# Performance work log

Hardware: AMD Instinct MI355X
Metric: run time of the kernel (lower is better)

The kernel has to match this reference:

```python
import jax, jax.numpy as jnp
import numpy as np

B, T, C, H = 2, 2048, 768, 12
HD = C // H  # head dim = 64
EPS = 1e-5


def layer_norm(x, g, b):
    mu = jnp.mean(x, axis=-1, keepdims=True)
    var = jnp.var(x, axis=-1, keepdims=True)
    return (x - mu) * jax.lax.rsqrt(var + EPS) * g + b


def setup_inputs() -> dict:
    key = jax.random.key(0)
    ks = jax.random.split(key, 5)
    s = 0.02
    return {
        "x": jax.random.normal(ks[0], (B, T, C), jnp.float32),
        "ln1_g": jnp.ones((C,), jnp.float32),
        "ln1_b": jnp.zeros((C,), jnp.float32),
        "W_qkv": jax.random.normal(ks[1], (C, 3 * C), jnp.float32) * s,
        "W_attn_proj": jax.random.normal(ks[2], (C, C), jnp.float32) * s,
        "ln2_g": jnp.ones((C,), jnp.float32),
        "ln2_b": jnp.zeros((C,), jnp.float32),
        "W_fc": jax.random.normal(ks[3], (C, 4 * C), jnp.float32) * s,
        "W_mlp_proj": jax.random.normal(ks[4], (4 * C, C), jnp.float32) * s,
    }


def attention(x, W_qkv, W_attn_proj):
    b, t, c = x.shape
    qkv = x @ W_qkv  # [B,T,3C]
    q, k, v = jnp.split(qkv, 3, axis=-1)
    # [B,H,T,HD]
    q = q.reshape(b, t, H, HD).transpose(0, 2, 1, 3)
    k = k.reshape(b, t, H, HD).transpose(0, 2, 1, 3)
    v = v.reshape(b, t, H, HD).transpose(0, 2, 1, 3)
    att = jnp.einsum("bhqd,bhkd->bhqk", q, k) * (1.0 / np.sqrt(HD).astype(np.float32))
    causal = jnp.tril(jnp.ones((t, t), jnp.bool_))
    att = jnp.where(causal, att, jnp.finfo(att.dtype).min)
    att = jax.nn.softmax(att, axis=-1)
    y = jnp.einsum("bhqk,bhkd->bhqd", att, v)
    y = y.transpose(0, 2, 1, 3).reshape(b, t, c)
    return y @ W_attn_proj


def mlp(x, W_fc, W_mlp_proj):
    h = jax.nn.gelu(x @ W_fc, approximate=False)
    return h @ W_mlp_proj


def reference(x, ln1_g, ln1_b, W_qkv, W_attn_proj, ln2_g, ln2_b, W_fc, W_mlp_proj):
    x = x + attention(layer_norm(x, ln1_g, ln1_b), W_qkv, W_attn_proj)
    x = x + mlp(layer_norm(x, ln2_g, ln2_b), W_fc, W_mlp_proj)
    return x
```

## Files before the change

kernel.cpp:

```cpp
#include <hip/hip_runtime.h>
#include <cstdint>
#include <cstddef>

typedef unsigned short u16;
typedef __attribute__((ext_vector_type(4))) float f32x4;
typedef __attribute__((ext_vector_type(8))) short bf16x8;

__device__ __forceinline__ u16 f2bf(float f) {
  unsigned int u = __builtin_bit_cast(unsigned int, f);
  u += 0x7fffu + ((u >> 16) & 1u);
  return (u16)(u >> 16);
}

__device__ __forceinline__ void gl_lds16(const u16* g, u16* lds_base) {
  __builtin_amdgcn_global_load_lds(
      (const __attribute__((address_space(1))) unsigned int*)g,
      (__attribute__((address_space(3))) unsigned int*)lds_base, 16, 0, 0);
}

__global__ __launch_bounds__(256) void transpose_all(const float* __restrict__ s0,
                                                     const float* __restrict__ s1,
                                                     const float* __restrict__ s2,
                                                     const float* __restrict__ s3,
                                                     u16* __restrict__ d0,
                                                     u16* __restrict__ d1,
                                                     u16* __restrict__ d2,
                                                     u16* __restrict__ d3) {
  __shared__ float tile[32][33];
  int idx = blockIdx.x;
  const float* src; u16* dst; int K, N, t;
  if (idx < 1728)      { src = s0; dst = d0; K = 768;  N = 2304; t = idx; }
  else if (idx < 2304) { src = s1; dst = d1; K = 768;  N = 768;  t = idx - 1728; }
  else if (idx < 4608) { src = s2; dst = d2; K = 768;  N = 3072; t = idx - 2304; }
  else                 { src = s3; dst = d3; K = 3072; N = 768;  t = idx - 4608; }
  int nt_n = N >> 5;
  int n0 = (t % nt_n) * 32, k0 = (t / nt_n) * 32;
  int tx = threadIdx.x & 31, ty = threadIdx.x >> 5;
#pragma unroll
  for (int i = 0; i < 4; ++i)
    tile[ty + i * 8][tx] = src[(size_t)(k0 + ty + i * 8) * N + n0 + tx];
  __syncthreads();
#pragma unroll
  for (int i = 0; i < 4; ++i)
    dst[(size_t)(n0 + ty + i * 8) * K + k0 + tx] = f2bf(tile[tx][ty + i * 8]);
}

__global__ __launch_bounds__(256) void transpose_v(const u16* __restrict__ qkvb,
                                                   u16* __restrict__ vt,
                                                   unsigned int* __restrict__ ctr) {
  __shared__ u16 tile[64 * 72];
  if (blockIdx.x == 0 && blockIdx.y == 0 && threadIdx.x == 0) *ctr = 0u;
  int t0 = blockIdx.x * 64;
  int bh = blockIdx.y;
  int b = bh / 12, h = bh % 12;
  int tid = threadIdx.x;
  int c8 = tid & 7, r = tid >> 3;
#pragma unroll
  for (int i = 0; i < 2; ++i) {
    int rr = r + i * 32;
    *(uint4*)&tile[rr * 72 + c8 * 8] =
        *(const uint4*)&qkvb[(size_t)(b * 2048 + t0 + rr) * 2304 + 1536 + h * 64 + c8 * 8];
  }
  __syncthreads();
#pragma unroll
  for (int i = 0; i < 2; ++i) {
    int dr = r + i * 32;
    u16 tmp[8];
#pragma unroll
    for (int j = 0; j < 8; ++j) tmp[j] = tile[(c8 * 8 + j) * 72 + dr];
    *(uint4*)&vt[((size_t)bh * 64 + dr) * 2048 + t0 + c8 * 8] = *(uint4*)tmp;
  }
}

__global__ __launch_bounds__(192) void ln_rows(const float* __restrict__ x,
                                               const float* __restrict__ g,
                                               const float* __restrict__ bb,
                                               u16* __restrict__ out) {
  int row = blockIdx.x;
  int t = threadIdx.x;
  float4 v = *(const float4*)(x + (size_t)row * 768 + t * 4);
  float s = v.x + v.y + v.z + v.w;
  float sq = v.x * v.x + v.y * v.y + v.z * v.z + v.w * v.w;
#pragma unroll
  for (int o = 32; o > 0; o >>= 1) {
    s += __shfl_down(s, o);
    sq += __shfl_down(sq, o);
  }
  __shared__ float ss[3], s2[3];
  int w = t >> 6;
  if ((t & 63) == 0) { ss[w] = s; s2[w] = sq; }
  __syncthreads();
  s = ss[0] + ss[1] + ss[2];
  sq = s2[0] + s2[1] + s2[2];
  float mu = s * (1.f / 768.f);
  float var = sq * (1.f / 768.f) - mu * mu;
  float rs = rsqrtf(var + 1e-5f);
  float4 gv = *(const float4*)(g + t * 4);
  float4 bv = *(const float4*)(bb + t * 4);
  u16 o4[4];
  o4[0] = f2bf((v.x - mu) * rs * gv.x + bv.x);
  o4[1] = f2bf((v.y - mu) * rs * gv.y + bv.y);
  o4[2] = f2bf((v.z - mu) * rs * gv.z + bv.z);
  o4[3] = f2bf((v.w - mu) * rs * gv.w + bv.w);
  *(uint2*)(out + (size_t)row * 768 + t * 4) = *(uint2*)o4;
}

template <int EPI, int CFG>
__global__ __launch_bounds__(256, (CFG == 0) ? 2 : 3)
void gemm_bt(const u16* __restrict__ A, const u16* __restrict__ BT,
             int M, int N, int K,
             float* __restrict__ outF, u16* __restrict__ outB,
             const float* __restrict__ res) {
  constexpr int TM = (CFG == 0) ? 128 : 64;
  constexpr int TN = (CFG == 0) ? 128 : 64;
  constexpr int MT = (CFG == 0) ? 4 : 1;
  __shared__ __align__(16) u16 Al[2][TM * 64];
  __shared__ __align__(16) u16 Bl[2][TN * 64];
  int tid = threadIdx.x;
  int lane = tid & 63, w = tid >> 6;
  int l16 = lane & 15, quad = lane >> 4;
  int swz = l16 & 7;
  int wrow = (CFG == 0) ? (w >> 1) * 64 : w * 16;
  int wcol = (CFG == 0) ? (w & 1) * 64 : 0;
  size_t rowA0 = (size_t)blockIdx.y * TM;
  size_t rowB0 = (size_t)blockIdx.x * TN;

  auto stage = [&](int buf, int k0) {
#pragma unroll
    for (int i = 0; i < TM / 32; ++i) {
      int cbase = (i * 4 + w) * 64;
      int chunk = cbase + lane;
      int r = chunk >> 3, c8 = (chunk & 7) ^ (r & 7);
      gl_lds16(&A[(rowA0 + r) * (size_t)K + k0 + c8 * 8], &Al[buf][cbase * 8]);
    }
#pragma unroll
    for (int i = 0; i < TN / 32; ++i) {
      int cbase = (i * 4 + w) * 64;
      int chunk = cbase + lane;
      int r = chunk >> 3, c8 = (chunk & 7) ^ (r & 7);
      gl_lds16(&BT[(rowB0 + r) * (size_t)K + k0 + c8 * 8], &Bl[buf][cbase * 8]);
    }
  };

  f32x4 acc[MT][4] = {};
  stage(0, 0);
  int cur = 0;
  for (int k0 = 0; k0 < K; k0 += 64) {
    __syncthreads();
    if (k0 + 64 < K) stage(cur ^ 1, k0 + 64);
#pragma unroll
    for (int ks = 0; ks < 2; ++ks) {
      int c = ks * 4 + quad;
      bf16x8 af[MT], bf[4];
#pragma unroll
      for (int mt = 0; mt < MT; ++mt)
        af[mt] = *(const bf16x8*)&Al[cur][(wrow + mt * 16 + l16) * 64 + (c ^ swz) * 8];
#pragma unroll
      for (int nt = 0; nt < 4; ++nt)
        bf[nt] = *(const bf16x8*)&Bl[cur][(wcol + nt * 16 + l16) * 64 + (c ^ swz) * 8];
#pragma unroll
      for (int mt = 0; mt < MT; ++mt)
#pragma unroll
        for (int nt = 0; nt < 4; ++nt)
          acc[mt][nt] = __builtin_amdgcn_mfma_f32_16x16x32_bf16(af[mt], bf[nt], acc[mt][nt], 0, 0, 0);
    }
    cur ^= 1;
  }

#pragma unroll
  for (int mt = 0; mt < MT; ++mt) {
#pragma unroll
    for (int i = 0; i < 4; ++i) {
      size_t row = rowA0 + wrow + mt * 16 + quad * 4 + i;
#pragma unroll
      for (int nt = 0; nt < 4; ++nt) {
        size_t col = rowB0 + wcol + nt * 16 + l16;
        float v = acc[mt][nt][i];
        if (EPI == 0) {
          outB[row * N + col] = f2bf(v);
        } else if (EPI == 1) {
          outF[row * N + col] = res[row * N + col] + v;
        } else {
          float ge = 0.5f * v * (1.f + erff(v * 0.70710678118654752f));
          outB[row * N + col] = f2bf(ge);
        }
      }
    }
  }
}

__global__ __launch_bounds__(256, 3) void flash_attn(const u16* __restrict__ qkv,
                                                     const u16* __restrict__ vt,
                                                     u16* __restrict__ y,
                                                     unsigned int* __restrict__ ctr) {
  __shared__ __align__(16) u16 Kl[2][64 * 64];
  __shared__ __align__(16) u16 Vl[2][64 * 64];
  __shared__ __align__(16) u16 Pl[4][16 * 72];
  __shared__ unsigned int s_unit;

  int tid = threadIdx.x;
  int lane = tid & 63, w = tid >> 6;
  int l16 = lane & 15, quad = lane >> 4;
  int swz = l16 & 7;
  u16* Pw = &Pl[w][0];
  const float sc = 0.125f * 1.44269504088896340736f;

  for (;;) {
    __syncthreads();
    if (tid == 0) s_unit = atomicAdd(ctr, 1u);
    __syncthreads();
    unsigned int u = s_unit;
    if (u >= 768u) return;

    int qt = 31 - (int)(u / 24u);
    int bh = (int)(u % 24u);
    int b = bh / 12, h = bh % 12;
    int qw = qt * 64 + w * 16;

    const u16* base = qkv + (size_t)b * 2048 * 2304;
    const u16* vbase = vt + (size_t)bh * 64 * 2048;

    auto stage = [&](int buf, int t0) {
#pragma unroll
      for (int i = 0; i < 2; ++i) {
        int cbase = (i * 4 + w) * 64;
        int chunk = cbase + lane;
        int r = chunk >> 3, c8 = (chunk & 7) ^ (r & 7);
        gl_lds16(base + (size_t)(t0 + r) * 2304 + 768 + h * 64 + c8 * 8, &Kl[buf][cbase * 8]);
      }
#pragma unroll
      for (int i = 0; i < 2; ++i) {
        int cbase = (i * 4 + w) * 64;
        int chunk = cbase + lane;
        int r = chunk >> 3, c8 = (chunk & 7) ^ (r & 7);
        gl_lds16(vbase + (size_t)r * 2048 + t0 + c8 * 8, &Vl[buf][cbase * 8]);
      }
    };

    bf16x8 qf0, qf1;
    {
      const u16* qp = base + (size_t)(qw + l16) * 2304 + h * 64 + quad * 8;
      qf0 = *(const bf16x8*)qp;
      qf1 = *(const bf16x8*)(qp + 32);
    }

    f32x4 O[4] = {};
    float l_i[4] = {0.f, 0.f, 0.f, 0.f};

    int nkb = qt + 1;
    stage(0, 0);
    int cur = 0;
    for (int kb = 0; kb < nkb; ++kb) {
      int kt0 = kb << 6;
      __syncthreads();
      if (kb + 1 < nkb) stage(cur ^ 1, kt0 + 64);

      f32x4 S[4];
#pragma unroll
      for (int nt = 0; nt < 4; ++nt) {
        bf16x8 k0 = *(const bf16x8*)&Kl[cur][(nt * 16 + l16) * 64 + (quad ^ swz) * 8];
        bf16x8 k1 = *(const bf16x8*)&Kl[cur][(nt * 16 + l16) * 64 + ((4 + quad) ^ swz) * 8];
        f32x4 z = {};
        z = __builtin_amdgcn_mfma_f32_16x16x32_bf16(qf0, k0, z, 0, 0, 0);
        S[nt] = __builtin_amdgcn_mfma_f32_16x16x32_bf16(qf1, k1, z, 0, 0, 0);
      }

      bool diag = (kb == nkb - 1);
#pragma unroll
      for (int nt = 0; nt < 4; ++nt) {
        int tk = kt0 + nt * 16 + l16;
#pragma unroll
        for (int i = 0; i < 4; ++i) {
          float p = exp2f(S[nt][i] * sc);
          if (diag && tk > qw + quad * 4 + i) p = 0.f;
          l_i[i] += p;
          Pw[(quad * 4 + i) * 72 + nt * 16 + l16] =
              (u16)(__builtin_bit_cast(unsigned int, p) >> 16);
        }
      }

      asm volatile("s_waitcnt lgkmcnt(0)" ::: "memory");

#pragma unroll
      for (int c = 0; c < 2; ++c) {
        bf16x8 pf = *(const bf16x8*)&Pw[l16 * 72 + c * 32 + quad * 8];
#pragma unroll
        for (int dt = 0; dt < 4; ++dt) {
          bf16x8 vf = *(const bf16x8*)&Vl[cur][(dt * 16 + l16) * 64 + ((c * 4 + quad) ^ swz) * 8];
          O[dt] = __builtin_amdgcn_mfma_f32_16x16x32_bf16(pf, vf, O[dt], 0, 0, 0);
        }
      }
      cur ^= 1;
    }

#pragma unroll
    for (int i = 0; i < 4; ++i) {
#pragma unroll
      for (int o = 1; o < 16; o <<= 1) l_i[i] += __shfl_xor(l_i[i], o);
    }
#pragma unroll
    for (int dt = 0; dt < 4; ++dt) {
#pragma unroll
      for (int i = 0; i < 4; ++i) {
        int tq = qw + quad * 4 + i;
        float ov = O[dt][i] / l_i[i];
        y[(size_t)(b * 2048 + tq) * 768 + h * 64 + dt * 16 + l16] = f2bf(ov);
      }
    }
  }
}

extern "C" void kernel_launch(void* const* d_in, const int* in_sizes, int n_in,
                              void* d_out, int out_size, void* d_ws, size_t ws_size,
                              hipStream_t stream) {
  const float* x      = (const float*)d_in[0];
  const float* ln1_g  = (const float*)d_in[1];
  const float* ln1_b  = (const float*)d_in[2];
  const float* W_qkv  = (const float*)d_in[3];
  const float* W_attn = (const float*)d_in[4];
  const float* ln2_g  = (const float*)d_in[5];
  const float* ln2_b  = (const float*)d_in[6];
  const float* W_fc   = (const float*)d_in[7];
  const float* W_mlp  = (const float*)d_in[8];
  float* out = (float*)d_out;

  const int M = 4096;
  char* p = (char*)d_ws;
  auto alloc = [&](size_t bytes) {
    char* r = p;
    p += (bytes + 255) & ~(size_t)255;
    return r;
  };
  u16* wt_qkv  = (u16*)alloc((size_t)2304 * 768 * 2);
  u16* wt_attn = (u16*)alloc((size_t)768 * 768 * 2);
  u16* wt_fc   = (u16*)alloc((size_t)3072 * 768 * 2);
  u16* wt_mlp  = (u16*)alloc((size_t)768 * 3072 * 2);
  u16* xn1     = (u16*)alloc((size_t)M * 768 * 2);
  u16* qkvb    = (u16*)alloc((size_t)M * 2304 * 2);
  u16* yb      = (u16*)alloc((size_t)M * 768 * 2);
  float* x1    = (float*)alloc((size_t)M * 768 * 4);
  u16* xn2     = (u16*)alloc((size_t)M * 768 * 2);
  u16* hb      = (u16*)alloc((size_t)M * 3072 * 2);
  u16* vt      = (u16*)alloc((size_t)24 * 64 * 2048 * 2);
  unsigned int* ctr = (unsigned int*)alloc(256);

  transpose_all<<<6912, 256, 0, stream>>>(W_qkv, W_attn, W_fc, W_mlp,
                                          wt_qkv, wt_attn, wt_fc, wt_mlp);

  ln_rows<<<M, 192, 0, stream>>>(x, ln1_g, ln1_b, xn1);
  gemm_bt<0, 0><<<dim3(2304 / 128, M / 128), 256, 0, stream>>>(xn1, wt_qkv, M, 2304, 768,
                                                               nullptr, qkvb, nullptr);
  transpose_v<<<dim3(32, 24), 256, 0, stream>>>(qkvb, vt, ctr);
  flash_attn<<<768, 256, 0, stream>>>(qkvb, vt, yb, ctr);
  gemm_bt<1, 1><<<dim3(768 / 64, M / 64), 256, 0, stream>>>(yb, wt_attn, M, 768, 768,
                                                            x1, nullptr, x);
  ln_rows<<<M, 192, 0, stream>>>(x1, ln2_g, ln2_b, xn2);
  gemm_bt<2, 0><<<dim3(3072 / 128, M / 128), 256, 0, stream>>>(xn2, wt_fc, M, 3072, 768,
                                                               nullptr, hb, nullptr);
  gemm_bt<1, 1><<<dim3(768 / 64, M / 64), 256, 0, stream>>>(hb, wt_mlp, M, 768, 3072,
                                                            out, nullptr, x1);
}
```

Measured before the change: 284.6 us.

## Use 128x64 GEMM tiles for QKV/FC and fold softmax scale into Q

The QKV and FC GEMMs move from 128x128 tiles to 128x64 tiles, with each wave owning 32 rows. This doubles the block count and allows three blocks per CU under the new launch bounds, at the cost of less B-tile reuse per block. The attention scale times log2(e) is now applied to the Q columns in the QKV GEMM epilogue, which removes a multiply per score in the flash attention inner loop. Q is therefore rounded to bf16 after scaling, which slightly changes numerics.

```diff
diff --git a/kernel.cpp b/kernel.cpp
--- a/kernel.cpp
+++ b/kernel.cpp
@@ -105,25 +105,22 @@
   *(uint2*)(out + (size_t)row * 768 + t * 4) = *(uint2*)o4;
 }
 
-template <int EPI, int CFG>
-__global__ __launch_bounds__(256, (CFG == 0) ? 2 : 3)
-void gemm_bt(const u16* __restrict__ A, const u16* __restrict__ BT,
-             int M, int N, int K,
-             float* __restrict__ outF, u16* __restrict__ outB,
-             const float* __restrict__ res) {
-  constexpr int TM = (CFG == 0) ? 128 : 64;
-  constexpr int TN = (CFG == 0) ? 128 : 64;
-  constexpr int MT = (CFG == 0) ? 4 : 1;
+template <int EPI, int TM, int QS>
+__global__ __launch_bounds__(256, 3) void gemm_bt(const u16* __restrict__ A,
+                                                  const u16* __restrict__ BT,
+                                                  int M, int N, int K,
+                                                  float* __restrict__ outF,
+                                                  u16* __restrict__ outB,
+                                                  const float* __restrict__ res) {
+  constexpr int MT = TM / 64;
   __shared__ __align__(16) u16 Al[2][TM * 64];
-  __shared__ __align__(16) u16 Bl[2][TN * 64];
+  __shared__ __align__(16) u16 Bl[2][64 * 64];
   int tid = threadIdx.x;
   int lane = tid & 63, w = tid >> 6;
   int l16 = lane & 15, quad = lane >> 4;
   int swz = l16 & 7;
-  int wrow = (CFG == 0) ? (w >> 1) * 64 : w * 16;
-  int wcol = (CFG == 0) ? (w & 1) * 64 : 0;
   size_t rowA0 = (size_t)blockIdx.y * TM;
-  size_t rowB0 = (size_t)blockIdx.x * TN;
+  size_t rowB0 = (size_t)blockIdx.x * 64;
 
   auto stage = [&](int buf, int k0) {
 #pragma unroll
@@ -134,7 +131,7 @@
       gl_lds16(&A[(rowA0 + r) * (size_t)K + k0 + c8 * 8], &Al[buf][cbase * 8]);
     }
 #pragma unroll
-    for (int i = 0; i < TN / 32; ++i) {
+    for (int i = 0; i < 2; ++i) {
       int cbase = (i * 4 + w) * 64;
       int chunk = cbase + lane;
       int r = chunk >> 3, c8 = (chunk & 7) ^ (r & 7);
@@ -154,10 +151,10 @@
       bf16x8 af[MT], bf[4];
 #pragma unroll
       for (int mt = 0; mt < MT; ++mt)
-        af[mt] = *(const bf16x8*)&Al[cur][(wrow + mt * 16 + l16) * 64 + (c ^ swz) * 8];
+        af[mt] = *(const bf16x8*)&Al[cur][(w * (TM / 4) + mt * 16 + l16) * 64 + (c ^ swz) * 8];
 #pragma unroll
       for (int nt = 0; nt < 4; ++nt)
-        bf[nt] = *(const bf16x8*)&Bl[cur][(wcol + nt * 16 + l16) * 64 + (c ^ swz) * 8];
+        bf[nt] = *(const bf16x8*)&Bl[cur][(nt * 16 + l16) * 64 + (c ^ swz) * 8];
 #pragma unroll
       for (int mt = 0; mt < MT; ++mt)
 #pragma unroll
@@ -171,12 +168,13 @@
   for (int mt = 0; mt < MT; ++mt) {
 #pragma unroll
     for (int i = 0; i < 4; ++i) {
-      size_t row = rowA0 + wrow + mt * 16 + quad * 4 + i;
+      size_t row = rowA0 + w * (TM / 4) + mt * 16 + quad * 4 + i;
 #pragma unroll
       for (int nt = 0; nt < 4; ++nt) {
-        size_t col = rowB0 + wcol + nt * 16 + l16;
+        size_t col = rowB0 + nt * 16 + l16;
         float v = acc[mt][nt][i];
         if (EPI == 0) {
+          if (QS && col < 768) v *= 0.18033688011112043f;
           outB[row * N + col] = f2bf(v);
         } else if (EPI == 1) {
           outF[row * N + col] = res[row * N + col] + v;
@@ -203,7 +201,6 @@
   int l16 = lane & 15, quad = lane >> 4;
   int swz = l16 & 7;
   u16* Pw = &Pl[w][0];
-  const float sc = 0.125f * 1.44269504088896340736f;
 
   for (;;) {
     __syncthreads();
@@ -271,7 +268,7 @@
         int tk = kt0 + nt * 16 + l16;
 #pragma unroll
         for (int i = 0; i < 4; ++i) {
-          float p = exp2f(S[nt][i] * sc);
+          float p = exp2f(S[nt][i]);
           if (diag && tk > qw + quad * 4 + i) p = 0.f;
           l_i[i] += p;
           Pw[(quad * 4 + i) * 72 + nt * 16 + l16] =
@@ -348,15 +345,15 @@
                                           wt_qkv, wt_attn, wt_fc, wt_mlp);
 
   ln_rows<<<M, 192, 0, stream>>>(x, ln1_g, ln1_b, xn1);
-  gemm_bt<0, 0><<<dim3(2304 / 128, M / 128), 256, 0, stream>>>(xn1, wt_qkv, M, 2304, 768,
-                                                               nullptr, qkvb, nullptr);
+  gemm_bt<0, 128, 1><<<dim3(2304 / 64, M / 128), 256, 0, stream>>>(
+      xn1, wt_qkv, M, 2304, 768, nullptr, qkvb, nullptr);
   transpose_v<<<dim3(32, 24), 256, 0, stream>>>(qkvb, vt, ctr);
   flash_attn<<<768, 256, 0, stream>>>(qkvb, vt, yb, ctr);
-  gemm_bt<1, 1><<<dim3(768 / 64, M / 64), 256, 0, stream>>>(yb, wt_attn, M, 768, 768,
-                                                            x1, nullptr, x);
+  gemm_bt<1, 64, 0><<<dim3(768 / 64, M / 64), 256, 0, stream>>>(
+      yb, wt_attn, M, 768, 768, x1, nullptr, x);
   ln_rows<<<M, 192, 0, stream>>>(x1, ln2_g, ln2_b, xn2);
-  gemm_bt<2, 0><<<dim3(3072 / 128, M / 128), 256, 0, stream>>>(xn2, wt_fc, M, 3072, 768,
-                                                               nullptr, hb, nullptr);
-  gemm_bt<1, 1><<<dim3(768 / 64, M / 64), 256, 0, stream>>>(hb, wt_mlp, M, 768, 3072,
-                                                            out, nullptr, x1);
-}
+  gemm_bt<2, 128, 0><<<dim3(3072 / 64, M / 128), 256, 0, stream>>>(
+      xn2, wt_fc, M, 3072, 768, nullptr, hb, nullptr);
+  gemm_bt<1, 64, 0><<<dim3(768 / 64, M / 64), 256, 0, stream>>>(
+      hb, wt_mlp, M, 768, 3072, out, nullptr, x1);
+}
```

Measured after the change: 274.6 us. -3.5%, faster.
